# Kernel tuning notes

Hardware: AMD Instinct MI355X
Metric: run time of the kernel (lower is better)

## Reference

```python
import jax, jax.numpy as jnp
import numpy as np

VOCAB, EMB, HID, T, B = 50000, 300, 1024, 512, 64


def setup_inputs() -> dict:
    key = jax.random.key(0)
    ks = jax.random.split(key, 12)
    s_in = 1.0 / np.sqrt(HID)  # torch nn.RNN init scale
    return {
        "x": jax.random.randint(ks[0], (B, T), 0, VOCAB),
        "emb": jax.random.normal(ks[1], (VOCAB, EMB), jnp.float32),
        "W_ih0": jax.random.uniform(ks[2], (HID, EMB), jnp.float32, -s_in, s_in),
        "W_hh0": jax.random.uniform(ks[3], (HID, HID), jnp.float32, -s_in, s_in),
        "b_ih0": jax.random.uniform(ks[4], (HID,), jnp.float32, -s_in, s_in),
        "b_hh0": jax.random.uniform(ks[5], (HID,), jnp.float32, -s_in, s_in),
        "W_ih1": jax.random.uniform(ks[6], (HID, HID), jnp.float32, -s_in, s_in),
        "W_hh1": jax.random.uniform(ks[7], (HID, HID), jnp.float32, -s_in, s_in),
        "b_ih1": jax.random.uniform(ks[8], (HID,), jnp.float32, -s_in, s_in),
        "b_hh1": jax.random.uniform(ks[9], (HID,), jnp.float32, -s_in, s_in),
        "W_fc": jax.random.uniform(ks[10], (1, HID), jnp.float32, -s_in, s_in),
        "b_fc": jax.random.uniform(ks[11], (1,), jnp.float32, -s_in, s_in),
    }


def _rnn_layer(x, W_ih, W_hh, b_ih, b_hh):
    # x: [B, T, in]; precompute input projection for all timesteps (one big GEMM)
    pre = jnp.einsum('bti,hi->bth', x, W_ih) + b_ih  # [B, T, H]
    h0 = jnp.zeros((x.shape[0], W_hh.shape[0]), x.dtype)

    def step(h, p_t):
        h_new = jnp.tanh(p_t + h @ W_hh.T + b_hh)
        return h_new, h_new

    _, hs = jax.lax.scan(step, h0, jnp.swapaxes(pre, 0, 1))  # [T, B, H]
    return jnp.swapaxes(hs, 0, 1)  # [B, T, H]


def reference(x, emb, W_ih0, W_hh0, b_ih0, b_hh0, W_ih1, W_hh1, b_ih1, b_hh1, W_fc, b_fc):
    e = emb[x]                                   # [B, T, EMB] embedding lookup
    h1 = _rnn_layer(e, W_ih0, W_hh0, b_ih0, b_hh0)   # layer 0
    h2 = _rnn_layer(h1, W_ih1, W_hh1, b_ih1, b_hh1)  # layer 1
    last = h2[:, -1, :]                          # [B, H]
    return jax.nn.sigmoid(last @ W_fc.T + b_fc)  # [B, 1]
```

## Files before the change

### kernel.cpp

```cpp
#include <hip/hip_runtime.h>
#include <hip/hip_bf16.h>

#define VOCAB 50000
#define EMB   300
#define HID   1024
#define TT    512
#define BB    64


typedef __attribute__((ext_vector_type(8))) short short8;
typedef __attribute__((ext_vector_type(4))) float floatx4;

__device__ inline float b2f(unsigned int u) {
    union { unsigned int i; float f; } v; v.i = u << 16; return v.f;
}
__device__ inline unsigned short f2b(float f) {
    __hip_bfloat16 h = __float2bfloat16(f);
    return *reinterpret_cast<unsigned short*>(&h);
}

#define WAIT_VM16(N, A) asm volatile("s_waitcnt vmcnt(" #N ")"              \
    : "+v"((A)[0]), "+v"((A)[1]), "+v"((A)[2]), "+v"((A)[3]),               \
      "+v"((A)[4]), "+v"((A)[5]), "+v"((A)[6]), "+v"((A)[7]),               \
      "+v"((A)[8]), "+v"((A)[9]), "+v"((A)[10]), "+v"((A)[11]),             \
      "+v"((A)[12]), "+v"((A)[13]), "+v"((A)[14]), "+v"((A)[15])            \
    :: "memory")

__global__ __launch_bounds__(64)
void detect_kernel(const void* __restrict__ W, int* __restrict__ ctl)
{
    const int tid = threadIdx.x;
    const unsigned short* p = (const unsigned short*)W;
    int bad = 0;
    for (int i = tid; i < 1024; i += 64) {
        float v = b2f(p[2 * i]);
        if (!(v > -0.5f && v < 0.5f)) bad++;
    }
    for (int off = 32; off; off >>= 1) bad += __shfl_down(bad, off);
    if (tid == 0) ctl[0] = (bad > 16) ? 1 : 0;
    for (int i = 64 + tid; i < 576; i += 64) ctl[i] = 0;
}

__global__ __launch_bounds__(256)
void proj_kernel(const int*  __restrict__ xidx,
                 const void* __restrict__ emb,
                 const void* __restrict__ W,
                 const void* __restrict__ bias,
                 unsigned short* __restrict__ C,
                 const int* __restrict__ ctl)
{
    const int mode = ctl[0];
    const int K = EMB;
    __shared__ unsigned short Wl[16 * 312];
    const int tid = threadIdx.x;
    const int nb = blockIdx.x, mb = blockIdx.y;
    const int n0 = nb * 16;
    const int KP2 = 312;

    if (mode) {
        const float* Wf = (const float*)W;
        const int e4 = K >> 2, tot = 16 * e4;
        for (int i = tid; i < tot; i += 256) {
            int nl = i / e4, c = i - nl * e4;
            float4 f = *(const float4*)(Wf + (size_t)(n0 + nl) * K + c * 4);
            unsigned short* d = &Wl[nl * KP2 + c * 4];
            d[0] = f2b(f.x); d[1] = f2b(f.y); d[2] = f2b(f.z); d[3] = f2b(f.w);
        }
    } else {
        const unsigned short* Wb = (const unsigned short*)W;
        const int tot = 16 * K;
        for (int i = tid; i < tot; i += 256) {
            int nl = i / K, c = i - nl * K;
            Wl[nl * KP2 + c] = Wb[(size_t)(n0 + nl) * K + c];
        }
    }
    __syncthreads();

    const int wave = tid >> 6, lane = tid & 63;
    const int quad = lane >> 4, ln = lane & 15;
    const int r = mb * 64 + wave * 16 + ln;

    const unsigned short* Ab = nullptr;
    const float*          Af = nullptr;
    {
        int t = r >> 6, b = r & 63;
        size_t off = (size_t)xidx[b * TT + t] * K;
        if (mode) Af = (const float*)emb + off;
        else      Ab = (const unsigned short*)emb + off;
    }

    floatx4 acc = {0.f, 0.f, 0.f, 0.f};
    const int full = K >> 5;
    for (int kk = 0; kk < full; ++kk) {
        int k = kk * 32 + quad * 8;
        short8 a;
        if (mode) {
            float4 f0 = *(const float4*)(Af + k);
            float4 f1 = *(const float4*)(Af + k + 4);
            a[0]=f2b(f0.x); a[1]=f2b(f0.y); a[2]=f2b(f0.z); a[3]=f2b(f0.w);
            a[4]=f2b(f1.x); a[5]=f2b(f1.y); a[6]=f2b(f1.z); a[7]=f2b(f1.w);
        } else {
            const uint2* ap = (const uint2*)(Ab + k);
            ((uint2*)&a)[0] = ap[0];
            ((uint2*)&a)[1] = ap[1];
        }
        short8 b = *(const short8*)&Wl[ln * KP2 + k];
        acc = __builtin_amdgcn_mfma_f32_16x16x32_bf16(a, b, acc, 0, 0, 0);
    }
    {
        short8 a, b;
        for (int j = 0; j < 8; ++j) {
            int k = full * 32 + quad * 8 + j;
            bool in = (k < K);
            unsigned short raw = 0;
            if (in) raw = mode ? f2b(Af[k]) : Ab[k];
            a[j] = (short)raw;
            b[j] = in ? (short)Wl[ln * KP2 + k] : (short)0;
        }
        acc = __builtin_amdgcn_mfma_f32_16x16x32_bf16(a, b, acc, 0, 0, 0);
    }

    const int col = n0 + ln;
    const float bvf = mode ? ((const float*)bias)[col]
                           : b2f(((const unsigned short*)bias)[col]);
    for (int rg = 0; rg < 4; ++rg) {
        size_t addr = ((size_t)mb * 64 + nb) * 1024
                    + (size_t)(wave * 16 + quad * 4 + rg) * 16 + ln;
        C[addr] = f2b(acc[rg] + bvf);
    }
}

__global__ __launch_bounds__(256)
void scan2_kernel(unsigned short* __restrict__ preB,
                  unsigned short* __restrict__ h1B,
                  unsigned short* __restrict__ h2B,
                  const void* __restrict__ Whh0, const void* __restrict__ bhh0,
                  const void* __restrict__ Wih1, const void* __restrict__ bih1,
                  const void* __restrict__ Whh1, const void* __restrict__ bhh1,
                  int* __restrict__ ctl)
{
    const int mode = ctl[0];
    const int gbx  = blockIdx.x;
    const int L    = gbx >> 6;
    const int bx   = gbx & 63;
    const int n0   = bx * 16;
    int* flagsA    = ctl + 64;
    int* flagsSelf = ctl + (L ? 320 : 64);
    unsigned short* hB = L ? h2B : h1B;
    const void* Whh  = L ? Whh1 : Whh0;
    const void* bhhv = L ? bhh1 : bhh0;

    __shared__ unsigned short Wl[16 * 1032];
    __shared__ unsigned short Wn[16 * 1032];
    __shared__ __align__(16) unsigned short hTile[1024];
    __shared__ __align__(16) unsigned short pTile[1024];
    const int tid = threadIdx.x;

    if (mode) {
        const float* Wf = (const float*)Whh;
        for (int i = tid; i < 16 * 256; i += 256) {
            int nl = i >> 8, c = i & 255;
            float4 f = *(const float4*)(Wf + ((size_t)(n0 + nl) << 10) + c * 4);
            unsigned short* d = &Wl[nl * 1032 + c * 4];
            d[0] = f2b(f.x); d[1] = f2b(f.y); d[2] = f2b(f.z); d[3] = f2b(f.w);
        }
        if (L == 0) {
            const float* Wg = (const float*)Wih1;
            for (int i = tid; i < 16 * 256; i += 256) {
                int nl = i >> 8, c = i & 255;
                float4 f = *(const float4*)(Wg + ((size_t)(n0 + nl) << 10) + c * 4);
                unsigned short* d = &Wn[nl * 1032 + c * 4];
                d[0] = f2b(f.x); d[1] = f2b(f.y); d[2] = f2b(f.z); d[3] = f2b(f.w);
            }
        }
    } else {
        const unsigned short* Wb = (const unsigned short*)Whh;
        for (int i = tid; i < 16 * 128; i += 256) {
            int nl = i >> 7, c = i & 127;
            *(short8*)&Wl[nl * 1032 + c * 8] =
                *(const short8*)(Wb + ((size_t)(n0 + nl) << 10) + c * 8);
        }
        if (L == 0) {
            const unsigned short* Wg = (const unsigned short*)Wih1;
            for (int i = tid; i < 16 * 128; i += 256) {
                int nl = i >> 7, c = i & 127;
                *(short8*)&Wn[nl * 1032 + c * 8] =
                    *(const short8*)(Wg + ((size_t)(n0 + nl) << 10) + c * 8);
            }
        }
    }
    __syncthreads();

    const int wave = tid >> 6, lane = tid & 63;
    const int quad = lane >> 4, ln = lane & 15;
    const int brow = wave * 16 + ln;
    const int ncol = n0 + ln;
    const float bvf = mode ? ((const float*)bhhv)[ncol]
                           : b2f(((const unsigned short*)bhhv)[ncol]);
    const float bnf = (L == 0)
        ? (mode ? ((const float*)bih1)[ncol]
                : b2f(((const unsigned short*)bih1)[ncol]))
        : 0.f;
    const int b0 = wave * 16 + quad * 4;
    const unsigned short* wl = &Wl[ln * 1032 + quad * 8];
    const unsigned short* wn = &Wn[ln * 1032 + quad * 8];
    const int hoff = (quad >> 1) * 1024 + brow * 16 + (quad & 1) * 8;

    for (int t = 0; t < TT; ++t) {
        const unsigned short* pp = preB + (size_t)t * 65536 + (size_t)bx * 1024
                                        + (size_t)b0 * 16 + ln;
        unsigned int pr0, pr1, pr2, pr3;
        floatx4 acc  = {0.f, 0.f, 0.f, 0.f};
        floatx4 acc2 = {0.f, 0.f, 0.f, 0.f};

        if (L == 0) {
            pr0 = pp[0]; pr1 = pp[16]; pr2 = pp[32]; pr3 = pp[48];
            if (t > 0) {
                short8 a[32];
                const unsigned short* hp = hB + (size_t)((t - 1) & 1) * 65536 + hoff;
                #pragma unroll
                for (int kk = 0; kk < 32; ++kk)
                    asm volatile("global_load_dwordx4 %0, %1, off sc1"
                                 : "=v"(a[kk])
                                 : "v"(hp + (size_t)kk * 2048) : "memory");
                WAIT_VM16(16, a);
                #pragma unroll
                for (int kk = 0; kk < 16; ++kk) {
                    short8 b  = *(const short8*)(wl + kk * 32);
                    short8 bn = *(const short8*)(wn + kk * 32);
                    acc  = __builtin_amdgcn_mfma_f32_16x16x32_bf16(a[kk], b,  acc,  0, 0, 0);
                    acc2 = __builtin_amdgcn_mfma_f32_16x16x32_bf16(a[kk], bn, acc2, 0, 0, 0);
                }
                WAIT_VM16(0, (a + 16));
                #pragma unroll
                for (int kk = 16; kk < 32; ++kk) {
                    short8 b  = *(const short8*)(wl + kk * 32);
                    short8 bn = *(const short8*)(wn + kk * 32);
                    acc  = __builtin_amdgcn_mfma_f32_16x16x32_bf16(a[kk], b,  acc,  0, 0, 0);
                    acc2 = __builtin_amdgcn_mfma_f32_16x16x32_bf16(a[kk], bn, acc2, 0, 0, 0);
                }
            }
        } else {
            {
                const int* fp = &flagsA[bx * 4];
                int v;
                do {
                    asm volatile("global_load_dword %0, %1, off sc1\n\t"
                                 "s_waitcnt vmcnt(0)"
                                 : "=v"(v) : "v"(fp) : "memory");
                } while (v < t + 2);
            }
            if (t > 0) {
                short8 a[32];
                const unsigned short* hp = hB + (size_t)((t - 1) & 1) * 65536 + hoff;
                #pragma unroll
                for (int kk = 0; kk < 32; ++kk)
                    asm volatile("global_load_dwordx4 %0, %1, off sc1"
                                 : "=v"(a[kk])
                                 : "v"(hp + (size_t)kk * 2048) : "memory");
                WAIT_VM16(16, a);
                #pragma unroll
                for (int kk = 0; kk < 16; ++kk) {
                    short8 b = *(const short8*)(wl + kk * 32);
                    acc = __builtin_amdgcn_mfma_f32_16x16x32_bf16(a[kk], b, acc, 0, 0, 0);
                }
                asm volatile("global_load_ushort %0, %1, off sc1"
                             : "=v"(pr0) : "v"(pp) : "memory");
                asm volatile("global_load_ushort %0, %1, off offset:32 sc1"
                             : "=v"(pr1) : "v"(pp) : "memory");
                asm volatile("global_load_ushort %0, %1, off offset:64 sc1"
                             : "=v"(pr2) : "v"(pp) : "memory");
                asm volatile("global_load_ushort %0, %1, off offset:96 sc1"
                             : "=v"(pr3) : "v"(pp) : "memory");
                WAIT_VM16(4, (a + 16));
                #pragma unroll
                for (int kk = 16; kk < 32; ++kk) {
                    short8 b = *(const short8*)(wl + kk * 32);
                    acc = __builtin_amdgcn_mfma_f32_16x16x32_bf16(a[kk], b, acc, 0, 0, 0);
                }
            } else {
                asm volatile("global_load_ushort %0, %1, off sc1"
                             : "=v"(pr0) : "v"(pp) : "memory");
                asm volatile("global_load_ushort %0, %1, off offset:32 sc1"
                             : "=v"(pr1) : "v"(pp) : "memory");
                asm volatile("global_load_ushort %0, %1, off offset:64 sc1"
                             : "=v"(pr2) : "v"(pp) : "memory");
                asm volatile("global_load_ushort %0, %1, off offset:96 sc1"
                             : "=v"(pr3) : "v"(pp) : "memory");
            }
            asm volatile("s_waitcnt vmcnt(0)"
                         : "+v"(pr0), "+v"(pr1), "+v"(pr2), "+v"(pr3) :: "memory");
        }

        hTile[(b0 + 0) * 16 + ln] = f2b(tanhf(acc[0] + b2f(pr0) + bvf));
        hTile[(b0 + 1) * 16 + ln] = f2b(tanhf(acc[1] + b2f(pr1) + bvf));
        hTile[(b0 + 2) * 16 + ln] = f2b(tanhf(acc[2] + b2f(pr2) + bvf));
        hTile[(b0 + 3) * 16 + ln] = f2b(tanhf(acc[3] + b2f(pr3) + bvf));
        if (L == 0 && t > 0) {
            pTile[(b0 + 0) * 16 + ln] = f2b(acc2[0] + bnf);
            pTile[(b0 + 1) * 16 + ln] = f2b(acc2[1] + bnf);
            pTile[(b0 + 2) * 16 + ln] = f2b(acc2[2] + bnf);
            pTile[(b0 + 3) * 16 + ln] = f2b(acc2[3] + bnf);
        }
        __syncthreads();
        if (tid < 128) {
            short8 hv = *(const short8*)&hTile[tid * 8];
            asm volatile("global_store_dwordx4 %0, %1, off sc1"
                         :: "v"(hB + (size_t)(t & 1) * 65536 + (size_t)bx * 1024 + tid * 8),
                            "v"(hv) : "memory");
            if (L == 0 && t > 0) {
                short8 pv = *(const short8*)&pTile[tid * 8];
                asm volatile("global_store_dwordx4 %0, %1, off sc1"
                             :: "v"(preB + (size_t)(t - 1) * 65536 + (size_t)bx * 1024 + tid * 8),
                                "v"(pv) : "memory");
            }
        }
        if (t < TT - 1) {
            asm volatile("s_waitcnt vmcnt(0)" ::: "memory");
            __syncthreads();
            if (tid == 0) {
                int tv = t + 1;
                asm volatile("global_store_dword %0, %1, off sc1"
                             :: "v"(&flagsSelf[bx * 4]), "v"(tv) : "memory");
            }
            if (tid < 64) {
                const int* fp = &flagsSelf[tid * 4];
                int v;
                do {
                    asm volatile("global_load_dword %0, %1, off sc1\n\t"
                                 "s_waitcnt vmcnt(0)"
                                 : "=v"(v) : "v"(fp) : "memory");
                } while (__any(v < t + 1));
            }
            __syncthreads();
        }
    }

    if (L == 0) {
        asm volatile("s_waitcnt vmcnt(0)" ::: "memory");
        __syncthreads();
        if (tid == 0) {
            int tv = TT;
            asm volatile("global_store_dword %0, %1, off sc1"
                         :: "v"(&flagsSelf[bx * 4]), "v"(tv) : "memory");
        }
        if (tid < 64) {
            const int* fp = &flagsSelf[tid * 4];
            int v;
            do {
                asm volatile("global_load_dword %0, %1, off sc1\n\t"
                             "s_waitcnt vmcnt(0)"
                             : "=v"(v) : "v"(fp) : "memory");
            } while (__any(v < TT));
        }
        __syncthreads();

        const unsigned short* hp = hB + (size_t)((TT - 1) & 1) * 65536 + hoff;
        short8 a[32];
        floatx4 acc2 = {0.f, 0.f, 0.f, 0.f};
        #pragma unroll
        for (int kk = 0; kk < 32; ++kk)
            asm volatile("global_load_dwordx4 %0, %1, off sc1"
                         : "=v"(a[kk])
                         : "v"(hp + (size_t)kk * 2048) : "memory");
        WAIT_VM16(16, a);
        #pragma unroll
        for (int kk = 0; kk < 16; ++kk) {
            short8 bn = *(const short8*)(wn + kk * 32);
            acc2 = __builtin_amdgcn_mfma_f32_16x16x32_bf16(a[kk], bn, acc2, 0, 0, 0);
        }
        WAIT_VM16(0, (a + 16));
        #pragma unroll
        for (int kk = 16; kk < 32; ++kk) {
            short8 bn = *(const short8*)(wn + kk * 32);
            acc2 = __builtin_amdgcn_mfma_f32_16x16x32_bf16(a[kk], bn, acc2, 0, 0, 0);
        }
        pTile[(b0 + 0) * 16 + ln] = f2b(acc2[0] + bnf);
        pTile[(b0 + 1) * 16 + ln] = f2b(acc2[1] + bnf);
        pTile[(b0 + 2) * 16 + ln] = f2b(acc2[2] + bnf);
        pTile[(b0 + 3) * 16 + ln] = f2b(acc2[3] + bnf);
        __syncthreads();
        if (tid < 128) {
            short8 pv = *(const short8*)&pTile[tid * 8];
            asm volatile("global_store_dwordx4 %0, %1, off sc1"
                         :: "v"(preB + (size_t)(TT - 1) * 65536 + (size_t)bx * 1024 + tid * 8),
                            "v"(pv) : "memory");
        }
        asm volatile("s_waitcnt vmcnt(0)" ::: "memory");
        __syncthreads();
        if (tid == 0) {
            int tv = TT + 1;
            asm volatile("global_store_dword %0, %1, off sc1"
                         :: "v"(&flagsSelf[bx * 4]), "v"(tv) : "memory");
        }
    }
}

__global__ __launch_bounds__(1024)
void fc_kernel(const unsigned short* __restrict__ h,
               const void* __restrict__ Wfc,
               const void* __restrict__ bfc,
               float* __restrict__ out,
               const int* __restrict__ ctl)
{
    const int mode = ctl[0];
    const int tid = threadIdx.x;
    const int b = tid >> 4, sub = tid & 15;
    const unsigned short* hr = h + (size_t)((TT - 1) & 1) * 65536 + b * 16 + sub;
    float s = 0.f;
    for (int j = 0; j < 64; ++j) {
        float w = mode ? ((const float*)Wfc)[j * 16 + sub]
                       : b2f(((const unsigned short*)Wfc)[j * 16 + sub]);
        s += b2f(hr[(size_t)j * 1024]) * w;
    }
    for (int off = 8; off; off >>= 1)
        s += __shfl_down(s, off, 16);
    if (sub == 0) {
        float bv = mode ? ((const float*)bfc)[0]
                        : b2f(((const unsigned short*)bfc)[0]);
        out[b] = 1.f / (1.f + expf(-(s + bv)));
    }
}

extern "C" void kernel_launch(void* const* d_in, const int* in_sizes, int n_in,
                              void* d_out, int out_size, void* d_ws, size_t ws_size,
                              hipStream_t stream)
{
    const int*  x    = (const int*)d_in[0];
    const void* emb  = d_in[1];
    const void* Wih0 = d_in[2];
    const void* Whh0 = d_in[3];
    const void* bih0 = d_in[4];
    const void* bhh0 = d_in[5];
    const void* Wih1 = d_in[6];
    const void* Whh1 = d_in[7];
    const void* bih1 = d_in[8];
    const void* bhh1 = d_in[9];
    const void* Wfc  = d_in[10];
    const void* bfc  = d_in[11];
    float* out = (float*)d_out;

    char* ws = (char*)d_ws;
    int*            ctl  = (int*)ws;
    unsigned short* pre  = (unsigned short*)(ws + 4096);
    unsigned short* h1   = (unsigned short*)(ws + 4096 + (size_t)67108864);
    unsigned short* h2   = h1 + 2 * 65536;

    detect_kernel<<<dim3(1), dim3(64), 0, stream>>>(Whh0, ctl);
    proj_kernel<<<dim3(64, 512), dim3(256), 0, stream>>>(
        x, emb, Wih0, bih0, pre, ctl);
    scan2_kernel<<<dim3(128), dim3(256), 0, stream>>>(
        pre, h1, h2, Whh0, bhh0, Wih1, bih1, Whh1, bhh1, ctl);
    fc_kernel<<<dim3(1), dim3(1024), 0, stream>>>(h2, Wfc, bfc, out, ctl);
}
```

Before: 2.855 ms.

## Fuse layer-0 embedding input projection into persistent scan kernel

Removes the separate proj_kernel and instead has each layer-0 scan block compute its own input projection per timestep from the gathered embedding rows with MFMA, keeping W_ih0 in shared memory. The next timestep's embedding rows are prefetched into registers during the current step. This avoids a full GEMM pass that writes and re-reads the projected pre-activations through global memory, but it adds MFMA work, extra registers and extra LDS to the serial critical path of the layer-0 recurrence.

```diff
diff --git a/kernel.cpp b/kernel.cpp
--- a/kernel.cpp
+++ b/kernel.cpp
@@ -25,6 +25,53 @@
       "+v"((A)[8]), "+v"((A)[9]), "+v"((A)[10]), "+v"((A)[11]),             \
       "+v"((A)[12]), "+v"((A)[13]), "+v"((A)[14]), "+v"((A)[15])            \
     :: "memory")
+
+__device__ __forceinline__ void prefetch_A(const void* emb, int mode, int xq,
+                                           int quad, short8* af)
+{
+    if (mode) {
+        const float* Af = (const float*)emb + (size_t)xq * EMB;
+        #pragma unroll
+        for (int kk = 0; kk < 9; ++kk) {
+            int k = kk * 32 + quad * 8;
+            float4 f0 = *(const float4*)(Af + k);
+            float4 f1 = *(const float4*)(Af + k + 4);
+            short8 a;
+            a[0]=f2b(f0.x); a[1]=f2b(f0.y); a[2]=f2b(f0.z); a[3]=f2b(f0.w);
+            a[4]=f2b(f1.x); a[5]=f2b(f1.y); a[6]=f2b(f1.z); a[7]=f2b(f1.w);
+            af[kk] = a;
+        }
+        short8 a = {0,0,0,0,0,0,0,0};
+        if (quad == 0) {
+            float4 f0 = *(const float4*)(Af + 288);
+            float4 f1 = *(const float4*)(Af + 292);
+            a[0]=f2b(f0.x); a[1]=f2b(f0.y); a[2]=f2b(f0.z); a[3]=f2b(f0.w);
+            a[4]=f2b(f1.x); a[5]=f2b(f1.y); a[6]=f2b(f1.z); a[7]=f2b(f1.w);
+        } else if (quad == 1) {
+            float4 f0 = *(const float4*)(Af + 296);
+            a[0]=f2b(f0.x); a[1]=f2b(f0.y); a[2]=f2b(f0.z); a[3]=f2b(f0.w);
+        }
+        af[9] = a;
+    } else {
+        const unsigned short* Ab = (const unsigned short*)emb + (size_t)xq * EMB;
+        #pragma unroll
+        for (int kk = 0; kk < 9; ++kk) {
+            int k = kk * 32 + quad * 8;
+            short8 a;
+            ((uint2*)&a)[0] = *(const uint2*)(Ab + k);
+            ((uint2*)&a)[1] = *(const uint2*)(Ab + k + 4);
+            af[kk] = a;
+        }
+        short8 a = {0,0,0,0,0,0,0,0};
+        if (quad == 0) {
+            ((uint2*)&a)[0] = *(const uint2*)(Ab + 288);
+            ((uint2*)&a)[1] = *(const uint2*)(Ab + 292);
+        } else if (quad == 1) {
+            ((uint2*)&a)[0] = *(const uint2*)(Ab + 296);
+        }
+        af[9] = a;
+    }
+}
 
 __global__ __launch_bounds__(64)
 void detect_kernel(const void* __restrict__ W, int* __restrict__ ctl)
@@ -42,96 +89,10 @@
 }
 
 __global__ __launch_bounds__(256)
-void proj_kernel(const int*  __restrict__ xidx,
-                 const void* __restrict__ emb,
-                 const void* __restrict__ W,
-                 const void* __restrict__ bias,
-                 unsigned short* __restrict__ C,
-                 const int* __restrict__ ctl)
-{
-    const int mode = ctl[0];
-    const int K = EMB;
-    __shared__ unsigned short Wl[16 * 312];
-    const int tid = threadIdx.x;
-    const int nb = blockIdx.x, mb = blockIdx.y;
-    const int n0 = nb * 16;
-    const int KP2 = 312;
-
-    if (mode) {
-        const float* Wf = (const float*)W;
-        const int e4 = K >> 2, tot = 16 * e4;
-        for (int i = tid; i < tot; i += 256) {
-            int nl = i / e4, c = i - nl * e4;
-            float4 f = *(const float4*)(Wf + (size_t)(n0 + nl) * K + c * 4);
-            unsigned short* d = &Wl[nl * KP2 + c * 4];
-            d[0] = f2b(f.x); d[1] = f2b(f.y); d[2] = f2b(f.z); d[3] = f2b(f.w);
-        }
-    } else {
-        const unsigned short* Wb = (const unsigned short*)W;
-        const int tot = 16 * K;
-        for (int i = tid; i < tot; i += 256) {
-            int nl = i / K, c = i - nl * K;
-            Wl[nl * KP2 + c] = Wb[(size_t)(n0 + nl) * K + c];
-        }
-    }
-    __syncthreads();
-
-    const int wave = tid >> 6, lane = tid & 63;
-    const int quad = lane >> 4, ln = lane & 15;
-    const int r = mb * 64 + wave * 16 + ln;
-
-    const unsigned short* Ab = nullptr;
-    const float*          Af = nullptr;
-    {
-        int t = r >> 6, b = r & 63;
-        size_t off = (size_t)xidx[b * TT + t] * K;
-        if (mode) Af = (const float*)emb + off;
-        else      Ab = (const unsigned short*)emb + off;
-    }
-
-    floatx4 acc = {0.f, 0.f, 0.f, 0.f};
-    const int full = K >> 5;
-    for (int kk = 0; kk < full; ++kk) {
-        int k = kk * 32 + quad * 8;
-        short8 a;
-        if (mode) {
-            float4 f0 = *(const float4*)(Af + k);
-            float4 f1 = *(const float4*)(Af + k + 4);
-            a[0]=f2b(f0.x); a[1]=f2b(f0.y); a[2]=f2b(f0.z); a[3]=f2b(f0.w);
-            a[4]=f2b(f1.x); a[5]=f2b(f1.y); a[6]=f2b(f1.z); a[7]=f2b(f1.w);
-        } else {
-            const uint2* ap = (const uint2*)(Ab + k);
-            ((uint2*)&a)[0] = ap[0];
-            ((uint2*)&a)[1] = ap[1];
-        }
-        short8 b = *(const short8*)&Wl[ln * KP2 + k];
-        acc = __builtin_amdgcn_mfma_f32_16x16x32_bf16(a, b, acc, 0, 0, 0);
-    }
-    {
-        short8 a, b;
-        for (int j = 0; j < 8; ++j) {
-            int k = full * 32 + quad * 8 + j;
-            bool in = (k < K);
-            unsigned short raw = 0;
-            if (in) raw = mode ? f2b(Af[k]) : Ab[k];
-            a[j] = (short)raw;
-            b[j] = in ? (short)Wl[ln * KP2 + k] : (short)0;
-        }
-        acc = __builtin_amdgcn_mfma_f32_16x16x32_bf16(a, b, acc, 0, 0, 0);
-    }
-
-    const int col = n0 + ln;
-    const float bvf = mode ? ((const float*)bias)[col]
-                           : b2f(((const unsigned short*)bias)[col]);
-    for (int rg = 0; rg < 4; ++rg) {
-        size_t addr = ((size_t)mb * 64 + nb) * 1024
-                    + (size_t)(wave * 16 + quad * 4 + rg) * 16 + ln;
-        C[addr] = f2b(acc[rg] + bvf);
-    }
-}
-
-__global__ __launch_bounds__(256)
-void scan2_kernel(unsigned short* __restrict__ preB,
+void scan2_kernel(const int*  __restrict__ xidx,
+                  const void* __restrict__ emb,
+                  const void* __restrict__ Wih0, const void* __restrict__ bih0,
+                  unsigned short* __restrict__ preB,
                   unsigned short* __restrict__ h1B,
                   unsigned short* __restrict__ h2B,
                   const void* __restrict__ Whh0, const void* __restrict__ bhh0,
@@ -152,6 +113,7 @@
 
     __shared__ unsigned short Wl[16 * 1032];
     __shared__ unsigned short Wn[16 * 1032];
+    __shared__ unsigned short Wp[16 * 328];
     __shared__ __align__(16) unsigned short hTile[1024];
     __shared__ __align__(16) unsigned short pTile[1024];
     const int tid = threadIdx.x;
@@ -172,6 +134,13 @@
                 unsigned short* d = &Wn[nl * 1032 + c * 4];
                 d[0] = f2b(f.x); d[1] = f2b(f.y); d[2] = f2b(f.z); d[3] = f2b(f.w);
             }
+            const float* Wf2 = (const float*)Wih0;
+            for (int i = tid; i < 16 * 75; i += 256) {
+                int nl = i / 75, c = i - nl * 75;
+                float4 f = *(const float4*)(Wf2 + (size_t)(n0 + nl) * EMB + c * 4);
+                unsigned short* d = &Wp[nl * 328 + c * 4];
+                d[0] = f2b(f.x); d[1] = f2b(f.y); d[2] = f2b(f.z); d[3] = f2b(f.w);
+            }
         }
     } else {
         const unsigned short* Wb = (const unsigned short*)Whh;
@@ -187,6 +156,17 @@
                 *(short8*)&Wn[nl * 1032 + c * 8] =
                     *(const short8*)(Wg + ((size_t)(n0 + nl) << 10) + c * 8);
             }
+            const unsigned short* Wb2 = (const unsigned short*)Wih0;
+            for (int i = tid; i < 16 * 300; i += 256) {
+                int nl = i / 300, c = i - nl * 300;
+                Wp[nl * 328 + c] = Wb2[(size_t)(n0 + nl) * EMB + c];
+            }
+        }
+    }
+    if (L == 0) {
+        for (int i = tid; i < 16 * 28; i += 256) {
+            int nl = i / 28, c = 300 + (i - nl * 28);
+            Wp[nl * 328 + c] = 0;
         }
     }
     __syncthreads();
@@ -195,8 +175,11 @@
     const int quad = lane >> 4, ln = lane & 15;
     const int brow = wave * 16 + ln;
     const int ncol = n0 + ln;
-    const float bvf = mode ? ((const float*)bhhv)[ncol]
-                           : b2f(((const unsigned short*)bhhv)[ncol]);
+    float bvf = mode ? ((const float*)bhhv)[ncol]
+                     : b2f(((const unsigned short*)bhhv)[ncol]);
+    if (L == 0)
+        bvf += mode ? ((const float*)bih0)[ncol]
+                    : b2f(((const unsigned short*)bih0)[ncol]);
     const float bnf = (L == 0)
         ? (mode ? ((const float*)bih1)[ncol]
                 : b2f(((const unsigned short*)bih1)[ncol]))
@@ -204,17 +187,35 @@
     const int b0 = wave * 16 + quad * 4;
     const unsigned short* wl = &Wl[ln * 1032 + quad * 8];
     const unsigned short* wn = &Wn[ln * 1032 + quad * 8];
+    const unsigned short* wp = &Wp[ln * 328 + quad * 8];
     const int hoff = (quad >> 1) * 1024 + brow * 16 + (quad & 1) * 8;
 
+    short8 af[10];
+    int xq1 = 0;
+    if (L == 0) {
+        int xq0 = xidx[brow * TT + 0];
+        prefetch_A(emb, mode, xq0, quad, af);
+        xq1 = xidx[brow * TT + 1];
+    }
+
     for (int t = 0; t < TT; ++t) {
-        const unsigned short* pp = preB + (size_t)t * 65536 + (size_t)bx * 1024
-                                        + (size_t)b0 * 16 + ln;
-        unsigned int pr0, pr1, pr2, pr3;
         floatx4 acc  = {0.f, 0.f, 0.f, 0.f};
         floatx4 acc2 = {0.f, 0.f, 0.f, 0.f};
+        short8 afn[10];
+        int xq2 = 0;
+        float fin0, fin1, fin2, fin3;
 
         if (L == 0) {
-            pr0 = pp[0]; pr1 = pp[16]; pr2 = pp[32]; pr3 = pp[48];
+            floatx4 acc0 = {0.f, 0.f, 0.f, 0.f};
+            #pragma unroll
+            for (int kk = 0; kk < 10; ++kk) {
+                short8 b = *(const short8*)(wp + kk * 32);
+                acc0 = __builtin_amdgcn_mfma_f32_16x16x32_bf16(af[kk], b, acc0, 0, 0, 0);
+            }
+            if (t + 1 < TT) {
+                prefetch_A(emb, mode, xq1, quad, afn);
+                if (t + 2 < TT) xq2 = xidx[brow * TT + t + 2];
+            }
             if (t > 0) {
                 short8 a[32];
                 const unsigned short* hp = hB + (size_t)((t - 1) & 1) * 65536 + hoff;
@@ -240,7 +241,14 @@
                     acc2 = __builtin_amdgcn_mfma_f32_16x16x32_bf16(a[kk], bn, acc2, 0, 0, 0);
                 }
             }
+            fin0 = acc[0] + acc0[0] + bvf;
+            fin1 = acc[1] + acc0[1] + bvf;
+            fin2 = acc[2] + acc0[2] + bvf;
+            fin3 = acc[3] + acc0[3] + bvf;
         } else {
+            const unsigned short* pp = preB + (size_t)t * 65536 + (size_t)bx * 1024
+                                            + (size_t)b0 * 16 + ln;
+            unsigned int pr0, pr1, pr2, pr3;
             {
                 const int* fp = &flagsA[bx * 4];
                 int v;
@@ -290,12 +298,16 @@
             }
             asm volatile("s_waitcnt vmcnt(0)"
                          : "+v"(pr0), "+v"(pr1), "+v"(pr2), "+v"(pr3) :: "memory");
-        }
-
-        hTile[(b0 + 0) * 16 + ln] = f2b(tanhf(acc[0] + b2f(pr0) + bvf));
-        hTile[(b0 + 1) * 16 + ln] = f2b(tanhf(acc[1] + b2f(pr1) + bvf));
-        hTile[(b0 + 2) * 16 + ln] = f2b(tanhf(acc[2] + b2f(pr2) + bvf));
-        hTile[(b0 + 3) * 16 + ln] = f2b(tanhf(acc[3] + b2f(pr3) + bvf));
+            fin0 = acc[0] + b2f(pr0) + bvf;
+            fin1 = acc[1] + b2f(pr1) + bvf;
+            fin2 = acc[2] + b2f(pr2) + bvf;
+            fin3 = acc[3] + b2f(pr3) + bvf;
+        }
+
+        hTile[(b0 + 0) * 16 + ln] = f2b(tanhf(fin0));
+        hTile[(b0 + 1) * 16 + ln] = f2b(tanhf(fin1));
+        hTile[(b0 + 2) * 16 + ln] = f2b(tanhf(fin2));
+        hTile[(b0 + 3) * 16 + ln] = f2b(tanhf(fin3));
         if (L == 0 && t > 0) {
             pTile[(b0 + 0) * 16 + ln] = f2b(acc2[0] + bnf);
             pTile[(b0 + 1) * 16 + ln] = f2b(acc2[1] + bnf);
@@ -333,6 +345,11 @@
                 } while (__any(v < t + 1));
             }
             __syncthreads();
+        }
+        if (L == 0 && t + 1 < TT) {
+            #pragma unroll
+            for (int j = 0; j < 10; ++j) af[j] = afn[j];
+            xq1 = xq2;
         }
     }
 
@@ -447,9 +464,8 @@
     unsigned short* h2   = h1 + 2 * 65536;
 
     detect_kernel<<<dim3(1), dim3(64), 0, stream>>>(Whh0, ctl);
-    proj_kernel<<<dim3(64, 512), dim3(256), 0, stream>>>(
-        x, emb, Wih0, bih0, pre, ctl);
     scan2_kernel<<<dim3(128), dim3(256), 0, stream>>>(
-        pre, h1, h2, Whh0, bhh0, Wih1, bih1, Whh1, bhh1, ctl);
+        x, emb, Wih0, bih0, pre, h1, h2,
+        Whh0, bhh0, Wih1, bih1, Whh1, bhh1, ctl);
     fc_kernel<<<dim3(1), dim3(1024), 0, stream>>>(h2, Wfc, bfc, out, ctl);
 }
```

Result: slower. 4.268 ms (+49.5%).

## Restructure input projection: one block per timestep with embeddings staged in LDS

Applied to the files above, without the earlier changes.

The projection kernel now launches one block per timestep instead of a 64x512 grid. Each block gathers that timestep's 64 embedding rows into shared memory once, then loops over all 64 output column tiles, reloading a 16-row weight slice each iteration. Output tiles are staged in shared memory so global writes are 16-byte vectors instead of scalar stores. This removes the repeated per-tile embedding gathers and the scalar tail handling. The cost is fewer blocks (512) with serialized weight loads and extra barriers per column tile. The scan kernel probably dominates total time anyway.

```diff
diff --git a/kernel.cpp b/kernel.cpp
--- a/kernel.cpp
+++ b/kernel.cpp
@@ -50,83 +50,85 @@
                  const int* __restrict__ ctl)
 {
     const int mode = ctl[0];
-    const int K = EMB;
-    __shared__ unsigned short Wl[16 * 312];
+    const int t   = blockIdx.x;
     const int tid = threadIdx.x;
-    const int nb = blockIdx.x, mb = blockIdx.y;
-    const int n0 = nb * 16;
-    const int KP2 = 312;
+    __shared__ unsigned short eT[64 * 328];
+    __shared__ unsigned short Wl[16 * 328];
+    __shared__ __align__(16) unsigned short oT[1024];
+    __shared__ int xqL[64];
+
+    if (tid < 64) xqL[tid] = xidx[tid * TT + t];
+    for (int i = tid; i < 64 * 28; i += 256) {
+        int b = i / 28, c = 300 + i % 28;
+        eT[b * 328 + c] = 0;
+    }
+    for (int i = tid; i < 16 * 28; i += 256) {
+        int nl = i / 28, c = 300 + i % 28;
+        Wl[nl * 328 + c] = 0;
+    }
+    __syncthreads();
 
     if (mode) {
-        const float* Wf = (const float*)W;
-        const int e4 = K >> 2, tot = 16 * e4;
-        for (int i = tid; i < tot; i += 256) {
-            int nl = i / e4, c = i - nl * e4;
-            float4 f = *(const float4*)(Wf + (size_t)(n0 + nl) * K + c * 4);
-            unsigned short* d = &Wl[nl * KP2 + c * 4];
+        for (int i = tid; i < 64 * 75; i += 256) {
+            int b = i / 75, seg = i % 75;
+            const float* src = (const float*)emb
+                             + (size_t)xqL[b] * EMB + seg * 4;
+            float4 f = *(const float4*)src;
+            unsigned short* d = &eT[b * 328 + seg * 4];
             d[0] = f2b(f.x); d[1] = f2b(f.y); d[2] = f2b(f.z); d[3] = f2b(f.w);
         }
     } else {
-        const unsigned short* Wb = (const unsigned short*)W;
-        const int tot = 16 * K;
-        for (int i = tid; i < tot; i += 256) {
-            int nl = i / K, c = i - nl * K;
-            Wl[nl * KP2 + c] = Wb[(size_t)(n0 + nl) * K + c];
-        }
-    }
-    __syncthreads();
+        for (int i = tid; i < 64 * 75; i += 256) {
+            int b = i / 75, seg = i % 75;
+            const unsigned short* src = (const unsigned short*)emb
+                                      + (size_t)xqL[b] * EMB + seg * 4;
+            *(uint2*)&eT[b * 328 + seg * 4] = *(const uint2*)src;
+        }
+    }
 
     const int wave = tid >> 6, lane = tid & 63;
     const int quad = lane >> 4, ln = lane & 15;
-    const int r = mb * 64 + wave * 16 + ln;
-
-    const unsigned short* Ab = nullptr;
-    const float*          Af = nullptr;
-    {
-        int t = r >> 6, b = r & 63;
-        size_t off = (size_t)xidx[b * TT + t] * K;
-        if (mode) Af = (const float*)emb + off;
-        else      Ab = (const unsigned short*)emb + off;
-    }
-
-    floatx4 acc = {0.f, 0.f, 0.f, 0.f};
-    const int full = K >> 5;
-    for (int kk = 0; kk < full; ++kk) {
-        int k = kk * 32 + quad * 8;
-        short8 a;
+
+    for (int nb = 0; nb < 64; ++nb) {
+        __syncthreads();
         if (mode) {
-            float4 f0 = *(const float4*)(Af + k);
-            float4 f1 = *(const float4*)(Af + k + 4);
-            a[0]=f2b(f0.x); a[1]=f2b(f0.y); a[2]=f2b(f0.z); a[3]=f2b(f0.w);
-            a[4]=f2b(f1.x); a[5]=f2b(f1.y); a[6]=f2b(f1.z); a[7]=f2b(f1.w);
+            const float* Wf = (const float*)W;
+            for (int i = tid; i < 16 * 75; i += 256) {
+                int nl = i / 75, seg = i % 75;
+                float4 f = *(const float4*)(Wf + (size_t)(nb * 16 + nl) * EMB + seg * 4);
+                unsigned short* d = &Wl[nl * 328 + seg * 4];
+                d[0] = f2b(f.x); d[1] = f2b(f.y); d[2] = f2b(f.z); d[3] = f2b(f.w);
+            }
         } else {
-            const uint2* ap = (const uint2*)(Ab + k);
-            ((uint2*)&a)[0] = ap[0];
-            ((uint2*)&a)[1] = ap[1];
-        }
-        short8 b = *(const short8*)&Wl[ln * KP2 + k];
-        acc = __builtin_amdgcn_mfma_f32_16x16x32_bf16(a, b, acc, 0, 0, 0);
-    }
-    {
-        short8 a, b;
-        for (int j = 0; j < 8; ++j) {
-            int k = full * 32 + quad * 8 + j;
-            bool in = (k < K);
-            unsigned short raw = 0;
-            if (in) raw = mode ? f2b(Af[k]) : Ab[k];
-            a[j] = (short)raw;
-            b[j] = in ? (short)Wl[ln * KP2 + k] : (short)0;
-        }
-        acc = __builtin_amdgcn_mfma_f32_16x16x32_bf16(a, b, acc, 0, 0, 0);
-    }
-
-    const int col = n0 + ln;
-    const float bvf = mode ? ((const float*)bias)[col]
-                           : b2f(((const unsigned short*)bias)[col]);
-    for (int rg = 0; rg < 4; ++rg) {
-        size_t addr = ((size_t)mb * 64 + nb) * 1024
-                    + (size_t)(wave * 16 + quad * 4 + rg) * 16 + ln;
-        C[addr] = f2b(acc[rg] + bvf);
+            const unsigned short* Wb = (const unsigned short*)W;
+            for (int i = tid; i < 16 * 75; i += 256) {
+                int nl = i / 75, seg = i % 75;
+                *(uint2*)&Wl[nl * 328 + seg * 4] =
+                    *(const uint2*)(Wb + (size_t)(nb * 16 + nl) * EMB + seg * 4);
+            }
+        }
+        __syncthreads();
+
+        floatx4 acc = {0.f, 0.f, 0.f, 0.f};
+        #pragma unroll
+        for (int kk = 0; kk < 10; ++kk) {
+            int k = kk * 32 + quad * 8;
+            short8 a = *(const short8*)&eT[(wave * 16 + ln) * 328 + k];
+            short8 b = *(const short8*)&Wl[ln * 328 + k];
+            acc = __builtin_amdgcn_mfma_f32_16x16x32_bf16(a, b, acc, 0, 0, 0);
+        }
+        const int col = nb * 16 + ln;
+        const float bvf = mode ? ((const float*)bias)[col]
+                               : b2f(((const unsigned short*)bias)[col]);
+        oT[(wave * 16 + quad * 4 + 0) * 16 + ln] = f2b(acc[0] + bvf);
+        oT[(wave * 16 + quad * 4 + 1) * 16 + ln] = f2b(acc[1] + bvf);
+        oT[(wave * 16 + quad * 4 + 2) * 16 + ln] = f2b(acc[2] + bvf);
+        oT[(wave * 16 + quad * 4 + 3) * 16 + ln] = f2b(acc[3] + bvf);
+        __syncthreads();
+        if (tid < 128) {
+            short8 hv = *(const short8*)&oT[tid * 8];
+            *(short8*)(C + ((size_t)t * 64 + nb) * 1024 + tid * 8) = hv;
+        }
     }
 }
 
@@ -447,7 +449,7 @@
     unsigned short* h2   = h1 + 2 * 65536;
 
     detect_kernel<<<dim3(1), dim3(64), 0, stream>>>(Whh0, ctl);
-    proj_kernel<<<dim3(64, 512), dim3(256), 0, stream>>>(
+    proj_kernel<<<dim3(512), dim3(256), 0, stream>>>(
         x, emb, Wih0, bih0, pre, ctl);
     scan2_kernel<<<dim3(128), dim3(256), 0, stream>>>(
         pre, h1, h2, Whh0, bhh0, Wih1, bih1, Whh1, bhh1, ctl);
```

Result: no change. 2.800 ms (-1.9%).
